# Kernel tuning notes

Measured on AMD Instinct MI355X. Metric: run time of the kernel, lower is better.

## Reference

```python
import jax, jax.numpy as jnp
import numpy as np

N_HEAD = 16

def setup_inputs() -> dict:
    key = jax.random.key(0)
    ks = jax.random.split(key, 4)
    B, T, C = 4, 2048, 1024
    x = jax.random.normal(ks[0], (B, T, C), dtype=jnp.float32)
    # causal mask: 1 where attendable (lower triangle), 0 elsewhere
    attn_mask = jnp.tril(jnp.ones((T, T), dtype=jnp.int32))[None, None, :, :]
    s = 0.02
    Wqkv = jax.random.normal(ks[1], (C, 3 * C), dtype=jnp.float32) * s
    bqkv = jnp.zeros((3 * C,), dtype=jnp.float32)
    Wout = jax.random.normal(ks[2], (C, C), dtype=jnp.float32) * s
    bout = jnp.zeros((C,), dtype=jnp.float32)
    return {"x": x, "attn_mask": attn_mask, "Wqkv": Wqkv, "bqkv": bqkv, "Wout": Wout, "bout": bout}

def reference(x, attn_mask, Wqkv, bqkv, Wout, bout):
    B, T, C = x.shape
    H = N_HEAD
    D = C // H
    qkv = x @ Wqkv + bqkv  # [B,T,3C]
    q, k, v = jnp.split(qkv, 3, axis=2)
    # [B,T,C] -> [B,H,T,D]
    q = q.reshape(B, T, H, D).transpose(0, 2, 1, 3)
    k = k.reshape(B, T, H, D).transpose(0, 2, 1, 3)
    v = v.reshape(B, T, H, D).transpose(0, 2, 1, 3)
    scores = jnp.einsum('bhqd,bhkd->bhqk', q, k) / jnp.sqrt(jnp.float32(D))
    scores = jnp.where(attn_mask == 0, jnp.float32(-jnp.inf), scores)
    probs = jax.nn.softmax(scores, axis=-1)  # dropout is identity in eval
    out = jnp.einsum('bhqk,bhkd->bhqd', probs, v)
    out = out.transpose(0, 2, 1, 3).reshape(B, T, C)
    return out @ Wout + bout
```

## Files before the change

### kernel.cpp

```cpp
#include <hip/hip_runtime.h>
#include <hip/hip_bf16.h>
#include <stdint.h>

#define TT 2048
#define CC 1024
#define HH 16
#define DD 64

typedef __bf16 bf16;
typedef bf16 bf16x8 __attribute__((ext_vector_type(8)));
typedef float f32x4 __attribute__((ext_vector_type(4)));
typedef float f32x16 __attribute__((ext_vector_type(16)));
typedef unsigned u32x4 __attribute__((ext_vector_type(4)));
typedef unsigned u32x2 __attribute__((ext_vector_type(2)));

#define MFMA16(a, b, c) __builtin_amdgcn_mfma_f32_16x16x32_bf16(a, b, c, 0, 0, 0)
#define MFMA32(a, b, c) __builtin_amdgcn_mfma_f32_32x32x16_bf16(a, b, c, 0, 0, 0)

#define SCLQ 0.18033688011112043f

typedef __attribute__((address_space(1))) unsigned int u32_g;
typedef __attribute__((address_space(3))) unsigned int u32_l;

__device__ __forceinline__ void gload_lds16(const void* g, void* l) {
  __builtin_amdgcn_global_load_lds((u32_g*)g, (u32_l*)l, 16, 0, 0);
}

__device__ __forceinline__ unsigned cvtpk(float a, float b) {
  unsigned r;
  asm("v_cvt_pk_bf16_f32 %0, %1, %2" : "=v"(r) : "v"(a), "v"(b));
  return r;
}

__device__ __forceinline__ void plswap(unsigned& a, unsigned& b) {
  asm("v_permlane32_swap_b32 %0, %1" : "+v"(a), "+v"(b));
}

__global__ __launch_bounds__(256) void k_cvt(const float* __restrict__ in,
                                             bf16* __restrict__ out, int n8) {
  int i = blockIdx.x * 256 + threadIdx.x;
  if (i >= n8) return;
  const float4* p = (const float4*)in + (size_t)i * 2;
  float4 a = p[0], b = p[1];
  bf16x8 o;
  o[0] = (bf16)a.x; o[1] = (bf16)a.y; o[2] = (bf16)a.z; o[3] = (bf16)a.w;
  o[4] = (bf16)b.x; o[5] = (bf16)b.y; o[6] = (bf16)b.z; o[7] = (bf16)b.w;
  *((bf16x8*)out + i) = o;
}

__global__ __launch_bounds__(256) void k_transpose_w(const float* __restrict__ in,
                                                     bf16* __restrict__ out,
                                                     int R, int C) {
  __shared__ float tile[64][65];
  int tcn = C >> 6;
  int tc = blockIdx.x % tcn;
  int tr = blockIdx.x / tcn;
  int t = threadIdx.x;
  int r0 = t >> 4;
  int cv = t & 15;
  const float4* src = (const float4*)(in + (size_t)(tr * 64) * C + tc * 64);
  int strideV = C >> 2;
#pragma unroll
  for (int p = 0; p < 4; ++p) {
    int r = r0 + p * 16;
    float4 v = src[(size_t)r * strideV + cv];
    tile[r][cv * 4 + 0] = v.x;
    tile[r][cv * 4 + 1] = v.y;
    tile[r][cv * 4 + 2] = v.z;
    tile[r][cv * 4 + 3] = v.w;
  }
  __syncthreads();
  int nn0 = t >> 3;
  int ck = t & 7;
#pragma unroll
  for (int p = 0; p < 2; ++p) {
    int nn = nn0 + p * 32;
    bf16x8 o;
#pragma unroll
    for (int i = 0; i < 8; ++i) o[i] = (bf16)tile[ck * 8 + i][nn];
    *(bf16x8*)(out + (size_t)(tc * 64 + nn) * R + tr * 64 + ck * 8) = o;
  }
}

template <int MODE>
__global__ __launch_bounds__(256) void k_gemm(const bf16* __restrict__ A,
                                              const bf16* __restrict__ Bt,
                                              int K, int N,
                                              const float* __restrict__ bias,
                                              bf16* __restrict__ Qd,
                                              bf16* __restrict__ Kd,
                                              bf16* __restrict__ Vd,
                                              float* __restrict__ Fd) {
  __shared__ __align__(16) char lds[32768];
  char* As = lds;
  char* Bs = lds + 16384;
  int nwg = gridDim.x;
  int bid = blockIdx.x;
  int cpx = nwg >> 3;
  int swz = (bid & 7) * cpx + (bid >> 3);
  int gx = N >> 7;
  int tm = swz / gx, tn = swz % gx;
  int wid = threadIdx.x >> 6, lane = threadIdx.x & 63;
  int wm = (wid >> 1) * 64, wn = (wid & 1) * 64;

  f32x4 acc[4][4];
#pragma unroll
  for (int i = 0; i < 4; ++i)
#pragma unroll
    for (int j = 0; j < 4; ++j) acc[i][j] = {0.f, 0.f, 0.f, 0.f};

  int arow[4], ain[4];
#pragma unroll
  for (int c = 0; c < 4; ++c) {
    int off = (wid * 4 + c) * 1024 + lane * 16;
    arow[c] = off >> 7;
    ain[c] = (off & 127) ^ ((arow[c] & 7) << 4);
  }

  for (int ks = 0; ks < K; ks += 64) {
    __syncthreads();
#pragma unroll
    for (int c = 0; c < 4; ++c) {
      gload_lds16(A + (size_t)(tm * 128 + arow[c]) * K + ks + (ain[c] >> 1),
                  As + (wid * 4 + c) * 1024);
      gload_lds16(Bt + (size_t)(tn * 128 + arow[c]) * K + ks + (ain[c] >> 1),
                  Bs + (wid * 4 + c) * 1024);
    }
    __syncthreads();
#pragma unroll
    for (int kk = 0; kk < 2; ++kk) {
      bf16x8 af[4], bfv[4];
      int inb = kk * 64 + (lane >> 4) * 16;
#pragma unroll
      for (int i = 0; i < 4; ++i) {
        int rowA = wm + i * 16 + (lane & 15);
        af[i] = *(const bf16x8*)(As + rowA * 128 + (inb ^ ((rowA & 7) << 4)));
        int rowB = wn + i * 16 + (lane & 15);
        bfv[i] = *(const bf16x8*)(Bs + rowB * 128 + (inb ^ ((rowB & 7) << 4)));
      }
#pragma unroll
      for (int i = 0; i < 4; ++i)
#pragma unroll
        for (int j = 0; j < 4; ++j) acc[i][j] = MFMA16(af[i], bfv[j], acc[i][j]);
    }
  }

  int r0 = (lane >> 4) * 4;
  int cn = lane & 15;
  if (MODE == 0) {
    int n0 = tn * 128 + wn;
    int which = n0 >> 10;
#pragma unroll
    for (int j = 0; j < 4; ++j) {
      int n = n0 + j * 16 + cn;
      float bv = bias[n];
      int h = (n >> 6) & 15;
      int d = n & 63;
#pragma unroll
      for (int i = 0; i < 4; ++i) {
#pragma unroll
        for (int r = 0; r < 4; ++r) {
          int m = tm * 128 + wm + i * 16 + r0 + r;
          int b = m >> 11, t = m & 2047;
          float val = acc[i][j][r] + bv;
          if (which == 0)
            Qd[(((size_t)(b * HH + h)) * TT + t) * DD + d] = (bf16)(val * SCLQ);
          else if (which == 1)
            Kd[(((size_t)(b * HH + h)) * TT + t) * DD + d] = (bf16)val;
          else
            Vd[(((size_t)(b * HH + h)) * DD + d) * TT + t] = (bf16)val;
        }
      }
    }
  } else {
#pragma unroll
    for (int j = 0; j < 4; ++j) {
      int n = tn * 128 + wn + j * 16 + cn;
      float bv = bias[n];
#pragma unroll
      for (int i = 0; i < 4; ++i) {
#pragma unroll
        for (int r = 0; r < 4; ++r) {
          int m = tm * 128 + wm + i * 16 + r0 + r;
          Fd[(size_t)m * N + n] = acc[i][j][r] + bv;
        }
      }
    }
  }
}

template <bool MASKED>
__device__ __forceinline__ void attn_tile(const char* __restrict__ sK,
                                          const char* __restrict__ sV,
                                          const bf16x8 qf[4],
                                          f32x16& o0, f32x16& o1, float& lrun,
                                          int base0, const int* __restrict__ colp,
                                          int hi, int qabs, int kvb) {
  f32x16 s0, s1;
#pragma unroll
  for (int g = 0; g < 16; ++g) { s0[g] = 0.f; s1[g] = 0.f; }
#pragma unroll
  for (int c = 0; c < 4; ++c) {
    bf16x8 kf0 = *(const bf16x8*)(sK + base0 + colp[c]);
    bf16x8 kf1 = *(const bf16x8*)(sK + base0 + 4096 + colp[c]);
    s0 = MFMA32(kf0, qf[c], s0);
    s1 = MFMA32(kf1, qf[c], s1);
  }
  float rs = 0.f;
#pragma unroll
  for (int g = 0; g < 16; ++g) {
    float p0 = __builtin_amdgcn_exp2f(s0[g]);
    float p1 = __builtin_amdgcn_exp2f(s1[g]);
    if (MASKED) {
      int kvr = (g & 3) + 8 * (g >> 2) + 4 * hi;
      p0 = (kvb + kvr <= qabs) ? p0 : 0.f;
      p1 = (kvb + 32 + kvr <= qabs) ? p1 : 0.f;
    }
    s0[g] = p0; s1[g] = p1;
    rs += p0 + p1;
  }
  lrun += rs;

  unsigned pk[8], qk[8];
#pragma unroll
  for (int i = 0; i < 8; ++i) {
    pk[i] = cvtpk(s0[2 * i], s0[2 * i + 1]);
    qk[i] = cvtpk(s1[2 * i], s1[2 * i + 1]);
  }
  plswap(pk[0], pk[2]); plswap(pk[1], pk[3]);
  plswap(pk[4], pk[6]); plswap(pk[5], pk[7]);
  plswap(qk[0], qk[2]); plswap(qk[1], qk[3]);
  plswap(qk[4], qk[6]); plswap(qk[5], qk[7]);

  bf16x8 pfr[4];
  pfr[0] = __builtin_bit_cast(bf16x8, (u32x4){pk[0], pk[1], pk[2], pk[3]});
  pfr[1] = __builtin_bit_cast(bf16x8, (u32x4){pk[4], pk[5], pk[6], pk[7]});
  pfr[2] = __builtin_bit_cast(bf16x8, (u32x4){qk[0], qk[1], qk[2], qk[3]});
  pfr[3] = __builtin_bit_cast(bf16x8, (u32x4){qk[4], qk[5], qk[6], qk[7]});

#pragma unroll
  for (int cc = 0; cc < 4; ++cc) {
    bf16x8 vf0 = *(const bf16x8*)(sV + base0 + colp[cc]);
    bf16x8 vf1 = *(const bf16x8*)(sV + base0 + 4096 + colp[cc]);
    o0 = MFMA32(vf0, pfr[cc], o0);
    o1 = MFMA32(vf1, pfr[cc], o1);
  }
}

__global__ __launch_bounds__(256) void k_attn(const bf16* __restrict__ Qg,
                                              const bf16* __restrict__ Kg,
                                              const bf16* __restrict__ Vtg,
                                              bf16* __restrict__ O) {
  __shared__ __align__(16) char lds[32768];

  int bid = blockIdx.x;
  int bh = (bid & 7) * 8 + ((bid >> 3) & 7);
  int pair = bid >> 6;
  int wid = threadIdx.x >> 6, lane = threadIdx.x & 63;
  int l31 = lane & 31, hi = lane >> 5;

  const bf16* Qh = Qg + (size_t)bh * TT * DD;
  const bf16* Kh = Kg + (size_t)bh * TT * DD;
  const bf16* Vh = Vtg + (size_t)bh * DD * TT;

  int base0 = l31 * 128;
  int colp[4];
#pragma unroll
  for (int c = 0; c < 4; ++c) colp[c] = (32 * c + 16 * hi) ^ ((l31 & 7) << 4);

  int soff[2], srow[2], scol[2];
#pragma unroll
  for (int c = 0; c < 2; ++c) {
    int off = (wid * 2 + c) * 1024 + lane * 16;
    soff[c] = (wid * 2 + c) * 1024;
    srow[c] = off >> 7;
    scol[c] = (off & 127) ^ ((srow[c] & 7) << 4);
  }

  int b = bh >> 4, h = bh & 15;

#pragma unroll 1
  for (int half = 0; half < 2; ++half) {
    int qt = half ? (15 - pair) : pair;
    int qb = qt * 128;
    int qw = qb + wid * 32;
    int qabs = qw + l31;

    bf16x8 qf[4];
#pragma unroll
    for (int c = 0; c < 4; ++c)
      qf[c] = *(const bf16x8*)(Qh + (size_t)qabs * DD + c * 16 + hi * 8);

    f32x16 o0, o1;
#pragma unroll
    for (int g = 0; g < 16; ++g) { o0[g] = 0.f; o1[g] = 0.f; }
    float lrun = 0.f;

    int ntile = 2 * qt + 2;

#pragma unroll
    for (int c = 0; c < 2; ++c) {
      gload_lds16(Kh + (size_t)srow[c] * DD + (scol[c] >> 1), lds + soff[c]);
      gload_lds16(Vh + (size_t)srow[c] * TT + (scol[c] >> 1), lds + 8192 + soff[c]);
    }
    __syncthreads();

    int cur = 0;
    for (int tk = 0; tk < ntile; ++tk) {
      int kvb = tk * 64;
      if (tk + 1 < ntile) {
        int kvn = kvb + 64;
        char* dK = lds + (cur ^ 1) * 16384;
        char* dV = dK + 8192;
#pragma unroll
        for (int c = 0; c < 2; ++c) {
          gload_lds16(Kh + (size_t)(kvn + srow[c]) * DD + (scol[c] >> 1), dK + soff[c]);
          gload_lds16(Vh + (size_t)srow[c] * TT + kvn + (scol[c] >> 1), dV + soff[c]);
        }
      }
      const char* sK = lds + cur * 16384;
      const char* sV = sK + 8192;
      if (kvb + 63 <= qw)
        attn_tile<false>(sK, sV, qf, o0, o1, lrun, base0, colp, hi, qabs, kvb);
      else if (kvb <= qw + 31)
        attn_tile<true>(sK, sV, qf, o0, o1, lrun, base0, colp, hi, qabs, kvb);
      __syncthreads();
      cur ^= 1;
    }

    lrun += __shfl_xor(lrun, 32);
    float rl = 1.0f / lrun;
    bf16* baseO = O + ((size_t)(b * TT + qabs)) * CC + h * 64;
#pragma unroll
    for (int G = 0; G < 4; ++G) {
      unsigned w0 = cvtpk(o0[4 * G] * rl, o0[4 * G + 1] * rl);
      unsigned w1 = cvtpk(o0[4 * G + 2] * rl, o0[4 * G + 3] * rl);
      *(u32x2*)(baseO + 8 * G + 4 * hi) = (u32x2){w0, w1};
      unsigned w2 = cvtpk(o1[4 * G] * rl, o1[4 * G + 1] * rl);
      unsigned w3 = cvtpk(o1[4 * G + 2] * rl, o1[4 * G + 3] * rl);
      *(u32x2*)(baseO + 32 + 8 * G + 4 * hi) = (u32x2){w2, w3};
    }
  }
}

extern "C" void kernel_launch(void* const* d_in, const int* in_sizes, int n_in,
                              void* d_out, int out_size, void* d_ws, size_t ws_size,
                              hipStream_t stream) {
  const float* x = (const float*)d_in[0];
  const float* Wqkv = (const float*)d_in[2];
  const float* bqkv = (const float*)d_in[3];
  const float* Wout = (const float*)d_in[4];
  const float* bout = (const float*)d_in[5];
  float* out = (float*)d_out;

  char* ws = (char*)d_ws;
  bf16* xb  = (bf16*)(ws);
  bf16* wt1 = (bf16*)(ws + (16u << 20));
  bf16* wt2 = (bf16*)(ws + (22u << 20));
  bf16* Qb  = (bf16*)(ws + (24u << 20));
  bf16* Kb  = (bf16*)(ws + (40u << 20));
  bf16* Vt  = (bf16*)(ws + (56u << 20));
  bf16* Ob  = (bf16*)(ws + (72u << 20));

  k_cvt<<<4096, 256, 0, stream>>>(x, xb, (4 * TT * CC) / 8);
  k_transpose_w<<<768, 256, 0, stream>>>(Wqkv, wt1, 1024, 3072);
  k_transpose_w<<<256, 256, 0, stream>>>(Wout, wt2, 1024, 1024);
  k_gemm<0><<<1536, 256, 0, stream>>>(xb, wt1, 1024, 3072, bqkv, Qb, Kb, Vt, nullptr);
  k_attn<<<512, 256, 0, stream>>>(Qb, Kb, Vt, Ob);
  k_gemm<1><<<512, 256, 0, stream>>>(Ob, wt2, 1024, 1024, bout, nullptr, nullptr, nullptr, out);
}
```

Measured before the change: 283.9 us.

## Use 256x128 GEMM tiles with triple-buffered async LDS prefetch

The projection GEMMs move to 512-thread blocks computing 256x128 output tiles, halving the grid. A three-stage LDS ring (144KB) prefetches K-tiles two steps ahead, using vmcnt waits and a single barrier per iteration in place of the two-barrier load-then-compute loop. MFMA issue is also wrapped in s_setprio. The aim is to hide global-load latency behind compute and raise B-tile reuse, at the cost of one workgroup per CU from the large LDS footprint and fewer blocks.

```diff
diff --git a/kernel.cpp b/kernel.cpp
--- a/kernel.cpp
+++ b/kernel.cpp
@@ -83,25 +83,25 @@
 }
 
 template <int MODE>
-__global__ __launch_bounds__(256) void k_gemm(const bf16* __restrict__ A,
+__global__ __launch_bounds__(512) void k_gemm(const bf16* __restrict__ A,
                                               const bf16* __restrict__ Bt,
-                                              int K, int N,
+                                              int Kdim, int N,
                                               const float* __restrict__ bias,
                                               bf16* __restrict__ Qd,
                                               bf16* __restrict__ Kd,
                                               bf16* __restrict__ Vd,
                                               float* __restrict__ Fd) {
-  __shared__ __align__(16) char lds[32768];
-  char* As = lds;
-  char* Bs = lds + 16384;
+  __shared__ __align__(16) char lds[147456];
   int nwg = gridDim.x;
   int bid = blockIdx.x;
   int cpx = nwg >> 3;
   int swz = (bid & 7) * cpx + (bid >> 3);
   int gx = N >> 7;
   int tm = swz / gx, tn = swz % gx;
-  int wid = threadIdx.x >> 6, lane = threadIdx.x & 63;
-  int wm = (wid >> 1) * 64, wn = (wid & 1) * 64;
+  int tid = threadIdx.x;
+  int wid = tid >> 6, lane = tid & 63;
+  int wm = (wid >> 1) * 64;
+  int wn = (wid & 1) * 64;
 
   f32x4 acc[4][4];
 #pragma unroll
@@ -109,39 +109,73 @@
 #pragma unroll
     for (int j = 0; j < 4; ++j) acc[i][j] = {0.f, 0.f, 0.f, 0.f};
 
-  int arow[4], ain[4];
-#pragma unroll
-  for (int c = 0; c < 4; ++c) {
-    int off = (wid * 4 + c) * 1024 + lane * 16;
-    arow[c] = off >> 7;
-    ain[c] = (off & 127) ^ ((arow[c] & 7) << 4);
-  }
-
-  for (int ks = 0; ks < K; ks += 64) {
-    __syncthreads();
-#pragma unroll
-    for (int c = 0; c < 4; ++c) {
-      gload_lds16(A + (size_t)(tm * 128 + arow[c]) * K + ks + (ain[c] >> 1),
-                  As + (wid * 4 + c) * 1024);
-      gload_lds16(Bt + (size_t)(tn * 128 + arow[c]) * K + ks + (ain[c] >> 1),
-                  Bs + (wid * 4 + c) * 1024);
-    }
-    __syncthreads();
+  int srow = tid >> 3;
+  int sinn = (((tid & 7) ^ ((tid >> 3) & 7)) << 4) >> 1;
+  int ldst = (tid & 7) << 4;
+  const bf16* Ab = A + (size_t)(tm * 256 + srow) * Kdim + sinn;
+  const bf16* Bb = Bt + (size_t)(tn * 128 + srow) * Kdim + sinn;
+
+  int NTt = Kdim >> 6;
+
+#pragma unroll
+  for (int t0 = 0; t0 < 2; ++t0) {
+    char* sa = lds + t0 * 49152;
+    char* sb = sa + 32768;
+    int ks = t0 * 64;
+#pragma unroll
+    for (int c = 0; c < 4; ++c)
+      gload_lds16(Ab + (size_t)(c * 64) * Kdim + ks, sa + c * 8192 + (tid >> 3) * 128 + ldst);
+#pragma unroll
+    for (int c = 0; c < 2; ++c)
+      gload_lds16(Bb + (size_t)(c * 64) * Kdim + ks, sb + c * 8192 + (tid >> 3) * 128 + ldst);
+  }
+
+  int fr = lane & 15;
+  int fx = ((lane >> 4) * 16) ^ ((lane & 7) << 4);
+
+#pragma unroll 1
+  for (int t = 0; t < NTt; ++t) {
+    if (t < NTt - 1)
+      asm volatile("s_waitcnt vmcnt(6)" ::: "memory");
+    else
+      asm volatile("s_waitcnt vmcnt(0)" ::: "memory");
+    __builtin_amdgcn_sched_barrier(0);
+    __builtin_amdgcn_s_barrier();
+    __builtin_amdgcn_sched_barrier(0);
+
+    if (t + 2 < NTt) {
+      int slot = t + 2;
+      while (slot >= 3) slot -= 3;
+      char* sa = lds + slot * 49152;
+      char* sb = sa + 32768;
+      int ks = (t + 2) * 64;
+#pragma unroll
+      for (int c = 0; c < 4; ++c)
+        gload_lds16(Ab + (size_t)(c * 64) * Kdim + ks, sa + c * 8192 + (tid >> 3) * 128 + ldst);
+#pragma unroll
+      for (int c = 0; c < 2; ++c)
+        gload_lds16(Bb + (size_t)(c * 64) * Kdim + ks, sb + c * 8192 + (tid >> 3) * 128 + ldst);
+    }
+
+    int cslot = t;
+    while (cslot >= 3) cslot -= 3;
+    const char* sa = lds + cslot * 49152;
+    const char* sb = sa + 32768;
 #pragma unroll
     for (int kk = 0; kk < 2; ++kk) {
       bf16x8 af[4], bfv[4];
-      int inb = kk * 64 + (lane >> 4) * 16;
+      int inb = kk * 64;
 #pragma unroll
       for (int i = 0; i < 4; ++i) {
-        int rowA = wm + i * 16 + (lane & 15);
-        af[i] = *(const bf16x8*)(As + rowA * 128 + (inb ^ ((rowA & 7) << 4)));
-        int rowB = wn + i * 16 + (lane & 15);
-        bfv[i] = *(const bf16x8*)(Bs + rowB * 128 + (inb ^ ((rowB & 7) << 4)));
+        af[i] = *(const bf16x8*)(sa + (wm + i * 16 + fr) * 128 + (inb ^ fx));
+        bfv[i] = *(const bf16x8*)(sb + (wn + i * 16 + fr) * 128 + (inb ^ fx));
       }
+      __builtin_amdgcn_s_setprio(1);
 #pragma unroll
       for (int i = 0; i < 4; ++i)
 #pragma unroll
         for (int j = 0; j < 4; ++j) acc[i][j] = MFMA16(af[i], bfv[j], acc[i][j]);
+      __builtin_amdgcn_s_setprio(0);
     }
   }
 
@@ -160,7 +194,7 @@
       for (int i = 0; i < 4; ++i) {
 #pragma unroll
         for (int r = 0; r < 4; ++r) {
-          int m = tm * 128 + wm + i * 16 + r0 + r;
+          int m = tm * 256 + wm + i * 16 + r0 + r;
           int b = m >> 11, t = m & 2047;
           float val = acc[i][j][r] + bv;
           if (which == 0)
@@ -181,7 +215,7 @@
       for (int i = 0; i < 4; ++i) {
 #pragma unroll
         for (int r = 0; r < 4; ++r) {
-          int m = tm * 128 + wm + i * 16 + r0 + r;
+          int m = tm * 256 + wm + i * 16 + r0 + r;
           Fd[(size_t)m * N + n] = acc[i][j][r] + bv;
         }
       }
@@ -365,7 +399,7 @@
   k_cvt<<<4096, 256, 0, stream>>>(x, xb, (4 * TT * CC) / 8);
   k_transpose_w<<<768, 256, 0, stream>>>(Wqkv, wt1, 1024, 3072);
   k_transpose_w<<<256, 256, 0, stream>>>(Wout, wt2, 1024, 1024);
-  k_gemm<0><<<1536, 256, 0, stream>>>(xb, wt1, 1024, 3072, bqkv, Qb, Kb, Vt, nullptr);
+  k_gemm<0><<<768, 512, 0, stream>>>(xb, wt1, 1024, 3072, bqkv, Qb, Kb, Vt, nullptr);
   k_attn<<<512, 256, 0, stream>>>(Qb, Kb, Vt, Ob);
-  k_gemm<1><<<512, 256, 0, stream>>>(Ob, wt2, 1024, 1024, bout, nullptr, nullptr, nullptr, out);
-}
+  k_gemm<1><<<256, 512, 0, stream>>>(Ob, wt2, 1024, 1024, bout, nullptr, nullptr, nullptr, out);
+}
```

Result: faster. 271.3 us (-4.4%).

## Rewrite projection GEMMs as 8-wave double-buffered kernels with larger tiles

Applied to the files above, without the earlier changes.

Replaces the 128x128 single-buffered GEMM with a 512-thread kernel using 256x256 tiles for the QKV projection and 128x256 for the output projection. Global-to-LDS loads are double-buffered and staggered across four compute phases, using explicit vmcnt waits, barriers and setprio so that loads overlap MFMA work. The larger tiles give more reuse per LDS byte, but only one workgroup fits per CU and the grids shrink to 384 and 256 blocks, which can leave CUs underfilled.

```diff
diff --git a/kernel.cpp b/kernel.cpp
--- a/kernel.cpp
+++ b/kernel.cpp
@@ -83,72 +83,149 @@
 }
 
 template <int MODE>
-__global__ __launch_bounds__(256) void k_gemm(const bf16* __restrict__ A,
-                                              const bf16* __restrict__ Bt,
-                                              int K, int N,
-                                              const float* __restrict__ bias,
-                                              bf16* __restrict__ Qd,
-                                              bf16* __restrict__ Kd,
-                                              bf16* __restrict__ Vd,
-                                              float* __restrict__ Fd) {
-  __shared__ __align__(16) char lds[32768];
-  char* As = lds;
-  char* Bs = lds + 16384;
+__global__ __launch_bounds__(512, 1) void k_gemm8(const bf16* __restrict__ A,
+                                                  const bf16* __restrict__ Bt,
+                                                  int Kd, int N,
+                                                  const float* __restrict__ bias,
+                                                  bf16* __restrict__ Qd,
+                                                  bf16* __restrict__ Kdst,
+                                                  bf16* __restrict__ Vd,
+                                                  float* __restrict__ Fd) {
+  constexpr int MREP = (MODE == 0) ? 8 : 4;
+  constexpr int BM = MREP * 32;
+  constexpr int ABYTES = BM * 128;
+  constexpr int BUF = ABYTES + 256 * 128;
+  __shared__ __align__(16) char lds[2 * BUF];
+
   int nwg = gridDim.x;
-  int bid = blockIdx.x;
-  int cpx = nwg >> 3;
-  int swz = (bid & 7) * cpx + (bid >> 3);
-  int gx = N >> 7;
+  int q8 = nwg >> 3;
+  int swz = (blockIdx.x & 7) * q8 + (blockIdx.x >> 3);
+  int gx = N >> 8;
   int tm = swz / gx, tn = swz % gx;
-  int wid = threadIdx.x >> 6, lane = threadIdx.x & 63;
-  int wm = (wid >> 1) * 64, wn = (wid & 1) * 64;
-
-  f32x4 acc[4][4];
-#pragma unroll
-  for (int i = 0; i < 4; ++i)
+  int tid = threadIdx.x, wid = tid >> 6, lane = tid & 63;
+  int wmr = (wid >> 2) * (BM / 2);
+  int wnr = (wid & 3) * 64;
+
+  f32x4 acc[MREP][4];
+#pragma unroll
+  for (int i = 0; i < MREP; ++i)
 #pragma unroll
     for (int j = 0; j < 4; ++j) acc[i][j] = {0.f, 0.f, 0.f, 0.f};
 
-  int arow[4], ain[4];
-#pragma unroll
-  for (int c = 0; c < 4; ++c) {
-    int off = (wid * 4 + c) * 1024 + lane * 16;
-    arow[c] = off >> 7;
-    ain[c] = (off & 127) ^ ((arow[c] & 7) << 4);
-  }
-
-  for (int ks = 0; ks < K; ks += 64) {
-    __syncthreads();
-#pragma unroll
-    for (int c = 0; c < 4; ++c) {
-      gload_lds16(A + (size_t)(tm * 128 + arow[c]) * K + ks + (ain[c] >> 1),
-                  As + (wid * 4 + c) * 1024);
-      gload_lds16(Bt + (size_t)(tn * 128 + arow[c]) * K + ks + (ain[c] >> 1),
-                  Bs + (wid * 4 + c) * 1024);
-    }
-    __syncthreads();
-#pragma unroll
-    for (int kk = 0; kk < 2; ++kk) {
-      bf16x8 af[4], bfv[4];
-      int inb = kk * 64 + (lane >> 4) * 16;
-#pragma unroll
-      for (int i = 0; i < 4; ++i) {
-        int rowA = wm + i * 16 + (lane & 15);
-        af[i] = *(const bf16x8*)(As + rowA * 128 + (inb ^ ((rowA & 7) << 4)));
-        int rowB = wn + i * 16 + (lane & 15);
-        bfv[i] = *(const bf16x8*)(Bs + rowB * 128 + (inb ^ ((rowB & 7) << 4)));
-      }
-#pragma unroll
-      for (int i = 0; i < 4; ++i)
-#pragma unroll
-        for (int j = 0; j < 4; ++j) acc[i][j] = MFMA16(af[i], bfv[j], acc[i][j]);
-    }
-  }
+  int urow = tid >> 3;
+  int ubyte = tid * 16;
+  int scole = (((tid & 7) ^ (urow & 7)) << 4) >> 1;
+  const bf16* Asrc = A + (size_t)(tm * BM + urow) * Kd + scole;
+  const bf16* Bsrc = Bt + (size_t)(tn * 256 + urow) * Kd + scole;
+
+#define STA(tt, qq, bb)                                               \
+  gload_lds16(Asrc + (size_t)((qq) * 64) * Kd + (tt) * 64,            \
+              lds + (bb) * BUF + (qq) * 8192 + ubyte)
+#define STB(tt, qq, bb)                                               \
+  gload_lds16(Bsrc + (size_t)((qq) * 64) * Kd + (tt) * 64,            \
+              lds + (bb) * BUF + ABYTES + (qq) * 8192 + ubyte)
+
+  int abase[MREP], bbase[4], col2[2];
+#pragma unroll
+  for (int i = 0; i < MREP; ++i) abase[i] = (wmr + i * 16 + (lane & 15)) * 128;
+#pragma unroll
+  for (int j = 0; j < 4; ++j) bbase[j] = ABYTES + (wnr + j * 16 + (lane & 15)) * 128;
+#pragma unroll
+  for (int s = 0; s < 2; ++s)
+    col2[s] = (s * 64 + ((lane >> 4) << 4)) ^ ((lane & 7) << 4);
+
+  int NT = Kd >> 6;
+
+  if constexpr (MODE == 0) {
+#pragma unroll
+    for (int q = 0; q < 4; ++q) { STA(0, q, 0); STB(0, q, 0); }
+    STA(1, 0, 1); STA(1, 2, 1); STB(1, 0, 1);
+    STB(1, 1, 1); STB(1, 2, 1); STB(1, 3, 1);
+    asm volatile("s_waitcnt vmcnt(6)" ::: "memory");
+  } else {
+    STA(0, 0, 0); STA(0, 1, 0);
+#pragma unroll
+    for (int q = 0; q < 4; ++q) STB(0, q, 0);
+#pragma unroll
+    for (int q = 0; q < 4; ++q) STB(1, q, 1);
+    asm volatile("s_waitcnt vmcnt(4)" ::: "memory");
+  }
+  __builtin_amdgcn_s_barrier();
+
+  bf16x8 breg[2][4];
+
+#define PHASE(g, s, STAGES, TAIL)                                              \
+  do {                                                                         \
+    bf16x8 afr[MREP / 2];                                                      \
+    if ((g) == 0) {                                                            \
+      _Pragma("unroll") for (int j = 0; j < 4; ++j)                            \
+          breg[s][j] = *(const bf16x8*)(cbuf + bbase[j] + col2[s]);            \
+    }                                                                          \
+    _Pragma("unroll") for (int i = 0; i < MREP / 2; ++i)                       \
+        afr[i] = *(const bf16x8*)(cbuf + abase[(g) * (MREP / 2) + i] + col2[s]); \
+    STAGES;                                                                    \
+    __builtin_amdgcn_s_barrier();                                              \
+    asm volatile("s_waitcnt lgkmcnt(0)" ::: "memory");                         \
+    __builtin_amdgcn_sched_barrier(0);                                         \
+    __builtin_amdgcn_s_setprio(1);                                             \
+    _Pragma("unroll") for (int i = 0; i < MREP / 2; ++i)                       \
+        _Pragma("unroll") for (int j = 0; j < 4; ++j)                          \
+            acc[(g) * (MREP / 2) + i][j] =                                     \
+                MFMA16(afr[i], breg[s][j], acc[(g) * (MREP / 2) + i][j]);      \
+    __builtin_amdgcn_s_setprio(0);                                             \
+    __builtin_amdgcn_sched_barrier(0);                                         \
+    TAIL;                                                                      \
+    __builtin_amdgcn_s_barrier();                                              \
+  } while (0)
+
+#pragma unroll 1
+  for (int t = 0; t < NT; ++t) {
+    int cur = t & 1;
+    const char* cbuf = lds + cur * BUF;
+
+    PHASE(0, 0,
+          {
+            if (t + 1 < NT) {
+              if constexpr (MODE == 0) { STA(t + 1, 1, cur ^ 1); STA(t + 1, 3, cur ^ 1); }
+              else { STA(t + 1, 0, cur ^ 1); STA(t + 1, 1, cur ^ 1); }
+            }
+          },
+          {});
+    PHASE(0, 1, {}, {});
+    PHASE(1, 0,
+          {
+            if (t + 2 < NT) {
+              if constexpr (MODE == 0) { STA(t + 2, 0, cur); STA(t + 2, 2, cur); STB(t + 2, 0, cur); }
+              else { STB(t + 2, 0, cur); STB(t + 2, 1, cur); }
+            }
+          },
+          {});
+    PHASE(1, 1,
+          {
+            if (t + 2 < NT) {
+              if constexpr (MODE == 0) { STB(t + 2, 1, cur); STB(t + 2, 2, cur); STB(t + 2, 3, cur); }
+              else { STB(t + 2, 2, cur); STB(t + 2, 3, cur); }
+            }
+          },
+          {
+            if (t + 1 < NT) {
+              if (t + 1 == NT - 1)
+                asm volatile("s_waitcnt vmcnt(0)" ::: "memory");
+              else if constexpr (MODE == 0)
+                asm volatile("s_waitcnt vmcnt(6)" ::: "memory");
+              else
+                asm volatile("s_waitcnt vmcnt(4)" ::: "memory");
+            }
+          });
+  }
+#undef PHASE
+#undef STA
+#undef STB
 
   int r0 = (lane >> 4) * 4;
   int cn = lane & 15;
-  if (MODE == 0) {
-    int n0 = tn * 128 + wn;
+  if constexpr (MODE == 0) {
+    int n0 = tn * 256 + wnr;
     int which = n0 >> 10;
 #pragma unroll
     for (int j = 0; j < 4; ++j) {
@@ -157,31 +234,31 @@
       int h = (n >> 6) & 15;
       int d = n & 63;
 #pragma unroll
-      for (int i = 0; i < 4; ++i) {
+      for (int i = 0; i < MREP; ++i) {
 #pragma unroll
         for (int r = 0; r < 4; ++r) {
-          int m = tm * 128 + wm + i * 16 + r0 + r;
-          int b = m >> 11, t = m & 2047;
+          int m = tm * BM + wmr + i * 16 + r0 + r;
+          int b = m >> 11, tt = m & 2047;
           float val = acc[i][j][r] + bv;
           if (which == 0)
-            Qd[(((size_t)(b * HH + h)) * TT + t) * DD + d] = (bf16)(val * SCLQ);
+            Qd[(((size_t)(b * HH + h)) * TT + tt) * DD + d] = (bf16)(val * SCLQ);
           else if (which == 1)
-            Kd[(((size_t)(b * HH + h)) * TT + t) * DD + d] = (bf16)val;
+            Kdst[(((size_t)(b * HH + h)) * TT + tt) * DD + d] = (bf16)val;
           else
-            Vd[(((size_t)(b * HH + h)) * DD + d) * TT + t] = (bf16)val;
+            Vd[(((size_t)(b * HH + h)) * DD + d) * TT + tt] = (bf16)val;
         }
       }
     }
   } else {
 #pragma unroll
     for (int j = 0; j < 4; ++j) {
-      int n = tn * 128 + wn + j * 16 + cn;
+      int n = tn * 256 + wnr + j * 16 + cn;
       float bv = bias[n];
 #pragma unroll
-      for (int i = 0; i < 4; ++i) {
+      for (int i = 0; i < MREP; ++i) {
 #pragma unroll
         for (int r = 0; r < 4; ++r) {
-          int m = tm * 128 + wm + i * 16 + r0 + r;
+          int m = tm * BM + wmr + i * 16 + r0 + r;
           Fd[(size_t)m * N + n] = acc[i][j][r] + bv;
         }
       }
@@ -365,7 +442,7 @@
   k_cvt<<<4096, 256, 0, stream>>>(x, xb, (4 * TT * CC) / 8);
   k_transpose_w<<<768, 256, 0, stream>>>(Wqkv, wt1, 1024, 3072);
   k_transpose_w<<<256, 256, 0, stream>>>(Wout, wt2, 1024, 1024);
-  k_gemm<0><<<1536, 256, 0, stream>>>(xb, wt1, 1024, 3072, bqkv, Qb, Kb, Vt, nullptr);
+  k_gemm8<0><<<384, 512, 0, stream>>>(xb, wt1, 1024, 3072, bqkv, Qb, Kb, Vt, nullptr);
   k_attn<<<512, 256, 0, stream>>>(Qb, Kb, Vt, Ob);
-  k_gemm<1><<<512, 256, 0, stream>>>(Ob, wt2, 1024, 1024, bout, nullptr, nullptr, nullptr, out);
-}
+  k_gemm8<1><<<256, 512, 0, stream>>>(Ob, wt2, 1024, 1024, bout, nullptr, nullptr, nullptr, out);
+}
```

New measurement: 286.7 us. About the same (+1.0%).
